# Kernel optimization log

Hardware: AMD Instinct MI355X
Metric: run time of the kernel (lower is better)

## Reference

```python
import jax, jax.numpy as jnp
import numpy as np

N, K, E = 20000, 4, 320000
IN_DIM, H_IN, D = 1024, 256, 128
GATE_IN = 2 * D + 1  # [h || m || logdeg]
GATE_H = 128         # max(d_out, 32)
TEMP = 0.6
M_CLAMP = 20.0


def _init(key, shape, fan_in):
    return jax.random.normal(key, shape, dtype=jnp.float32) / np.sqrt(fan_in)


def setup_inputs() -> dict:
    key = jax.random.key(0)
    ks = jax.random.split(key, 24)
    inp = {}
    inp['X'] = jax.random.normal(ks[0], (N, IN_DIM), dtype=jnp.float32)
    inp['rows'] = jax.random.randint(ks[1], (K, E), 0, N, dtype=jnp.int32)
    inp['cols'] = jax.random.randint(ks[2], (K, E), 0, N, dtype=jnp.int32)
    inp['mask'] = jnp.ones((N, K), dtype=jnp.float32)
    inp['logdeg'] = jax.random.uniform(ks[3], (N, K), dtype=jnp.float32) * 3.0
    # lin_in: 3-layer MLP 1024 -> 256 -> 256 -> 128, each + ReLU
    inp['W_in0'] = _init(ks[4], (IN_DIM, H_IN), IN_DIM); inp['b_in0'] = jnp.zeros((H_IN,), jnp.float32)
    inp['W_in1'] = _init(ks[5], (H_IN, H_IN), H_IN);     inp['b_in1'] = jnp.zeros((H_IN,), jnp.float32)
    inp['W_in2'] = _init(ks[6], (H_IN, D), H_IN);        inp['b_in2'] = jnp.zeros((D,), jnp.float32)
    # block 0
    inp['Wmsg0'] = _init(ks[7], (D, D), D)
    inp['Wg1_0'] = _init(ks[8], (GATE_IN, GATE_H), GATE_IN); inp['bg1_0'] = jnp.zeros((GATE_H,), jnp.float32)
    inp['Wg2_0'] = _init(ks[9], (GATE_H, 1), GATE_H);        inp['bg2_0'] = jnp.zeros((1,), jnp.float32)
    # block 1
    inp['Wmsg1'] = _init(ks[10], (D, D), D)
    inp['Wg1_1'] = _init(ks[11], (GATE_IN, GATE_H), GATE_IN); inp['bg1_1'] = jnp.zeros((GATE_H,), jnp.float32)
    inp['Wg2_1'] = _init(ks[12], (GATE_H, 1), GATE_H);        inp['bg2_1'] = jnp.zeros((1,), jnp.float32)
    # head
    inp['Wh1'] = _init(ks[13], (D, D), D); inp['bh1'] = jnp.zeros((D,), jnp.float32)
    inp['Wh2'] = _init(ks[14], (D, 1), D); inp['bh2'] = jnp.zeros((1,), jnp.float32)
    return inp


def reference(X, rows, cols, mask, logdeg,
              W_in0, b_in0, W_in1, b_in1, W_in2, b_in2,
              Wmsg0, Wg1_0, bg1_0, Wg2_0, bg2_0,
              Wmsg1, Wg1_1, bg1_1, Wg2_1, bg2_1,
              Wh1, bh1, Wh2, bh2):
    relu = jax.nn.relu
    # input encoder (eval mode: dropout / featdrop are identity)
    H = relu(relu(relu(X @ W_in0 + b_in0) @ W_in1 + b_in1) @ W_in2 + b_in2)

    def pairnorm(x):
        x = x - x.mean(axis=0, keepdims=True)
        mean_norm = jnp.sqrt(jnp.mean(jnp.sum(x * x, axis=1))) + 1e-6
        return x / mean_norm

    def block(H, Wmsg, Wg1, bg1, Wg2, bg2):
        Z = H @ Wmsg  # [N, D]
        def prop(r, c):  # sparse A_k @ Z with binary adjacency: out[r] += Z[c]
            return jax.ops.segment_sum(Z[c], r, num_segments=N)
        M = jnp.transpose(jax.vmap(prop)(rows, cols), (1, 0, 2))  # [N, K, D]
        M = jnp.clip(M, -M_CLAMP, M_CLAMP)
        H_rep = jnp.broadcast_to(H[:, None, :], (N, K, H.shape[1]))
        gate_in = jnp.concatenate([H_rep, M, logdeg[:, :, None]], axis=2)  # [N, K, 2D+1]
        scores = (relu(gate_in @ Wg1 + bg1) @ Wg2 + bg2)[..., 0]  # [N, K]
        alpha = jax.nn.softmax(scores / TEMP, axis=1)
        alpha = alpha * mask
        alpha = alpha / jnp.maximum(alpha.sum(axis=1, keepdims=True), 1e-12)
        alpha = jnp.maximum(alpha, 1e-8)
        alpha = alpha / jnp.maximum(alpha.sum(axis=1, keepdims=True), 1e-12)
        fused = jnp.einsum('nk,nkd->nd', alpha, M)
        return fused, alpha

    fused0, a0 = block(H, Wmsg0, Wg1_0, bg1_0, Wg2_0, bg2_0)
    H = relu(pairnorm(fused0 + H))
    fused1, a1 = block(H, Wmsg1, Wg1_1, bg1_1, Wg2_1, bg2_1)
    H = relu(pairnorm(fused1 + H))

    h = relu(relu(H) @ Wh1 + bh1)
    logits = (h @ Wh2 + bh2)[:, 0]  # [N]
    return logits, jnp.stack([a0, a1], axis=0)
```

## Files before the change

### kernel.cpp

```cpp
#include <hip/hip_runtime.h>
#include <hip/hip_bf16.h>

#define N_NODES 20000
#define KADJ 4
#define NEDGE 320000
#define ETOTAL (KADJ * NEDGE)
#define IN_DIM_ 1024
#define H_IN_ 256
#define DDIM 128
#define GATE_H_ 128
#define TEMP_ 0.6f
#define M_CLAMP_ 20.0f
#define CSR_TOTAL (KADJ * N_NODES)
#define NCOARSE 128
#define QPER (CSR_TOTAL / NCOARSE)
#define ESTRIDE 12288
#define TILE_A 4096
#define BINA_NB ((ETOTAL + TILE_A - 1) / TILE_A)

typedef __attribute__((ext_vector_type(8))) short frag_ab;
typedef __attribute__((ext_vector_type(4))) float frag_cd;
typedef __attribute__((ext_vector_type(8))) unsigned short us8;

__device__ inline unsigned short f2bf(float f) {
    unsigned int u = __float_as_uint(f);
    u += 0x7FFFu + ((u >> 16) & 1);
    return (unsigned short)(u >> 16);
}
__device__ inline float bflo(unsigned int p) { return __uint_as_float(p << 16); }
__device__ inline float bfhi(unsigned int p) { return __uint_as_float(p & 0xffff0000u); }

__device__ __forceinline__ void gld16(const unsigned short* g, unsigned short* l) {
    __builtin_amdgcn_global_load_lds(
        (const __attribute__((address_space(1))) void*)g,
        (__attribute__((address_space(3))) void*)l, 16, 0, 0);
}

__global__ __launch_bounds__(256) void cast_bf16_kernel(
    const float* __restrict__ X, unsigned short* __restrict__ Xb, int n)
{
    int i = (blockIdx.x * 256 + threadIdx.x) * 8;
    if (i >= n) return;
    float4 a = *(const float4*)(X + i), b = *(const float4*)(X + i + 4);
    us8 o;
    o[0] = f2bf(a.x); o[1] = f2bf(a.y); o[2] = f2bf(a.z); o[3] = f2bf(a.w);
    o[4] = f2bf(b.x); o[5] = f2bf(b.y); o[6] = f2bf(b.z); o[7] = f2bf(b.w);
    *(us8*)(Xb + i) = o;
}

#define PIPE_WAIT_NEXT()  asm volatile("s_waitcnt vmcnt(5)" ::: "memory")
#define PIPE_WAIT_LAST()  asm volatile("s_waitcnt vmcnt(0)" ::: "memory")
#define PIPE_BAR()        __builtin_amdgcn_s_barrier()
#define PIPE_FENCE()      __builtin_amdgcn_sched_barrier(0)


__global__ __launch_bounds__(256) void gemm_async_kernel(
    const unsigned short* __restrict__ A, const unsigned short* __restrict__ Bt,
    const float* __restrict__ bias, float* __restrict__ Cf, unsigned short* __restrict__ Cb,
    int M, int N, int K, int do_relu)
{
    __shared__ unsigned short sA[2][32 * 64];
    __shared__ unsigned short sB[2][128 * 64];
    int tid = threadIdx.x;
    int tileM = blockIdx.y * 32, tileN = blockIdx.x * 128;
    int w = tid >> 6, lane = tid & 63;
    int wr = (w & 1) * 16, wc = (w >> 1) * 64;
    int fm = lane & 15, fq = lane >> 4;
    int crow = lane >> 3;
    int gsw = (lane & 7) ^ crow;

    frag_cd acc[4] = {};

    auto stage = [&](int buf, int k0) {
        {
            int row = w * 8 + crow;
            int ar = min(tileM + row, M - 1);
            gld16(A + (size_t)ar * K + k0 + gsw * 8, &sA[buf][w * 512]);
        }
#pragma unroll
        for (int t = 0; t < 4; t++) {
            int chunk = w * 4 + t;
            int row = chunk * 8 + crow;
            gld16(Bt + (size_t)(tileN + row) * K + k0 + gsw * 8, &sB[buf][chunk * 512]);
        }
    };

    int nt = K >> 6;
    stage(0, 0);
    for (int t = 0; t < nt; t++) {
        int cur = t & 1;
        if (t + 1 < nt) { stage(cur ^ 1, (t + 1) << 6); PIPE_WAIT_NEXT(); }
        else            { PIPE_WAIT_LAST(); }
        PIPE_BAR();
        PIPE_FENCE();
#pragma unroll
        for (int s = 0; s < 2; s++) {
            int sw = ((s * 4 + fq) ^ (fm & 7)) * 8;
            frag_ab af = *(const frag_ab*)&sA[cur][(wr + fm) * 64 + sw];
#pragma unroll
            for (int j = 0; j < 4; j++) {
                frag_ab bf = *(const frag_ab*)&sB[cur][(wc + j * 16 + fm) * 64 + sw];
                acc[j] = __builtin_amdgcn_mfma_f32_16x16x32_bf16(af, bf, acc[j], 0, 0, 0);
            }
        }
        PIPE_FENCE();
        PIPE_BAR();
    }
    int row = tileM + wr + fq * 4;
#pragma unroll
    for (int r = 0; r < 4; r++) {
        if (row + r < M) {
#pragma unroll
            for (int j = 0; j < 4; j++) {
                int col = tileN + wc + j * 16 + fm;
                float v = acc[j][r];
                if (bias) v += bias[col];
                if (do_relu) v = fmaxf(v, 0.f);
                if (Cf) Cf[(size_t)(row + r) * N + col] = v;
                if (Cb) Cb[(size_t)(row + r) * N + col] = f2bf(v);
            }
        }
    }
}

__global__ __launch_bounds__(256) void zg_gemm_kernel(
    const unsigned short* __restrict__ A, const unsigned short* __restrict__ Bt,
    const float* __restrict__ bg1, unsigned short* __restrict__ Zb,
    float* __restrict__ GH, int M)
{
    __shared__ unsigned short sA[2][32 * 64];
    __shared__ unsigned short sB[2][128 * 64];
    int tid = threadIdx.x;
    int tileM = blockIdx.y * 32, tileN = blockIdx.x * 128;
    int w = tid >> 6, lane = tid & 63;
    int wr = (w & 1) * 16, wc = (w >> 1) * 64;
    int fm = lane & 15, fq = lane >> 4;
    int crow = lane >> 3;
    int gsw = (lane & 7) ^ crow;

    frag_cd acc[4] = {};

    auto stage = [&](int buf, int k0) {
        {
            int row = w * 8 + crow;
            int ar = min(tileM + row, M - 1);
            gld16(A + (size_t)ar * DDIM + k0 + gsw * 8, &sA[buf][w * 512]);
        }
#pragma unroll
        for (int t = 0; t < 4; t++) {
            int chunk = w * 4 + t;
            int row = chunk * 8 + crow;
            gld16(Bt + (size_t)(tileN + row) * DDIM + k0 + gsw * 8, &sB[buf][chunk * 512]);
        }
    };

    stage(0, 0);
#pragma unroll
    for (int t = 0; t < 2; t++) {
        int cur = t & 1;
        if (t == 0) { stage(1, 64); PIPE_WAIT_NEXT(); }
        else        { PIPE_WAIT_LAST(); }
        PIPE_BAR();
        PIPE_FENCE();
#pragma unroll
        for (int s = 0; s < 2; s++) {
            int sw = ((s * 4 + fq) ^ (fm & 7)) * 8;
            frag_ab af = *(const frag_ab*)&sA[cur][(wr + fm) * 64 + sw];
#pragma unroll
            for (int j = 0; j < 4; j++) {
                frag_ab bf = *(const frag_ab*)&sB[cur][(wc + j * 16 + fm) * 64 + sw];
                acc[j] = __builtin_amdgcn_mfma_f32_16x16x32_bf16(af, bf, acc[j], 0, 0, 0);
            }
        }
        PIPE_FENCE();
        PIPE_BAR();
    }
    int isZ = (blockIdx.x == 0);
    int row = tileM + wr + fq * 4;
#pragma unroll
    for (int r = 0; r < 4; r++) {
        if (row + r < M) {
#pragma unroll
            for (int j = 0; j < 4; j++) {
                int col = wc + j * 16 + fm;
                float v = acc[j][r];
                if (isZ) Zb[(size_t)(row + r) * DDIM + col] = f2bf(v);
                else     GH[(size_t)(row + r) * GATE_H_ + col] = v + bg1[col];
            }
        }
    }
}

__global__ __launch_bounds__(256) void head_gemm_kernel(
    const unsigned short* __restrict__ A, const unsigned short* __restrict__ Bt,
    const float* __restrict__ bh1, const float* __restrict__ Wh2,
    const float* __restrict__ bh2, float* __restrict__ logits, int M)
{
    __shared__ unsigned short sA[2][32 * 64];
    __shared__ unsigned short sB[2][128 * 64];
    __shared__ float sred[2][32];
    int tid = threadIdx.x;
    int tileM = blockIdx.x * 32;
    int w = tid >> 6, lane = tid & 63;
    int wr = (w & 1) * 16, wc = (w >> 1) * 64;
    int fm = lane & 15, fq = lane >> 4;
    int crow = lane >> 3;
    int gsw = (lane & 7) ^ crow;

    frag_cd acc[4] = {};

    auto stage = [&](int buf, int k0) {
        {
            int row = w * 8 + crow;
            int ar = min(tileM + row, M - 1);
            gld16(A + (size_t)ar * DDIM + k0 + gsw * 8, &sA[buf][w * 512]);
        }
#pragma unroll
        for (int t = 0; t < 4; t++) {
            int chunk = w * 4 + t;
            int row = chunk * 8 + crow;
            gld16(Bt + (size_t)row * DDIM + k0 + gsw * 8, &sB[buf][chunk * 512]);
        }
    };

    stage(0, 0);
#pragma unroll
    for (int t = 0; t < 2; t++) {
        int cur = t & 1;
        if (t == 0) { stage(1, 64); PIPE_WAIT_NEXT(); }
        else        { PIPE_WAIT_LAST(); }
        PIPE_BAR();
        PIPE_FENCE();
#pragma unroll
        for (int s = 0; s < 2; s++) {
            int sw = ((s * 4 + fq) ^ (fm & 7)) * 8;
            frag_ab af = *(const frag_ab*)&sA[cur][(wr + fm) * 64 + sw];
#pragma unroll
            for (int j = 0; j < 4; j++) {
                frag_ab bf = *(const frag_ab*)&sB[cur][(wc + j * 16 + fm) * 64 + sw];
                acc[j] = __builtin_amdgcn_mfma_f32_16x16x32_bf16(af, bf, acc[j], 0, 0, 0);
            }
        }
        PIPE_FENCE();
        PIPE_BAR();
    }
    float wv[4], bh[4];
#pragma unroll
    for (int j = 0; j < 4; j++) {
        int c = wc + j * 16 + fm;
        wv[j] = Wh2[c];
        bh[j] = bh1[c];
    }
    float part[4];
#pragma unroll
    for (int r = 0; r < 4; r++) {
        float p = 0.f;
#pragma unroll
        for (int j = 0; j < 4; j++) {
            float v = fmaxf(acc[j][r] + bh[j], 0.f);
            p += v * wv[j];
        }
        part[r] = p;
    }
#pragma unroll
    for (int m = 1; m < 16; m <<= 1)
#pragma unroll
        for (int r = 0; r < 4; r++)
            part[r] += __shfl_xor(part[r], m, 64);
    if (fm == 0) {
#pragma unroll
        for (int r = 0; r < 4; r++)
            sred[w >> 1][wr + fq * 4 + r] = part[r];
    }
    __syncthreads();
    if (tid < 32 && tileM + tid < M)
        logits[tileM + tid] = sred[0][tid] + sred[1][tid] + bh2[0];
}

__global__ __launch_bounds__(256) void gate_gemm_kernel(
    const unsigned short* __restrict__ Mb, const unsigned short* __restrict__ Bt,
    const float* __restrict__ GH, const float* __restrict__ logdeg,
    const float* __restrict__ wld, const float* __restrict__ Wg2,
    const float* __restrict__ bg2, float* __restrict__ scores)
{
    __shared__ unsigned short sA[2][32 * 64];
    __shared__ unsigned short sB[2][128 * 64];
    __shared__ float sred[2][32];
    int tid = threadIdx.x;
    int tile0 = blockIdx.x * 32;
    int w = tid >> 6, lane = tid & 63;
    int wr = (w & 1) * 16, wc = (w >> 1) * 64;
    int fm = lane & 15, fq = lane >> 4;
    int crow = lane >> 3;
    int gsw = (lane & 7) ^ crow;

    frag_cd acc[4] = {};

    auto stage = [&](int buf, int k0) {
        {
            int row = w * 8 + crow;
            gld16(Mb + (size_t)(tile0 + row) * DDIM + k0 + gsw * 8, &sA[buf][w * 512]);
        }
#pragma unroll
        for (int t = 0; t < 4; t++) {
            int chunk = w * 4 + t;
            int row = chunk * 8 + crow;
            gld16(Bt + (size_t)row * DDIM + k0 + gsw * 8, &sB[buf][chunk * 512]);
        }
    };

    stage(0, 0);
#pragma unroll
    for (int t = 0; t < 2; t++) {
        int cur = t & 1;
        if (t == 0) { stage(1, 64); PIPE_WAIT_NEXT(); }
        else        { PIPE_WAIT_LAST(); }
        PIPE_BAR();
        PIPE_FENCE();
#pragma unroll
        for (int s = 0; s < 2; s++) {
            int sw = ((s * 4 + fq) ^ (fm & 7)) * 8;
            frag_ab af = *(const frag_ab*)&sA[cur][(wr + fm) * 64 + sw];
#pragma unroll
            for (int j = 0; j < 4; j++) {
                frag_ab bf = *(const frag_ab*)&sB[cur][(wc + j * 16 + fm) * 64 + sw];
                acc[j] = __builtin_amdgcn_mfma_f32_16x16x32_bf16(af, bf, acc[j], 0, 0, 0);
            }
        }
        PIPE_FENCE();
        PIPE_BAR();
    }
    float wg2v[4], wldv[4];
#pragma unroll
    for (int j = 0; j < 4; j++) {
        int c = wc + j * 16 + fm;
        wg2v[j] = Wg2[c];
        wldv[j] = wld[c];
    }
    float part[4];
#pragma unroll
    for (int r = 0; r < 4; r++) {
        int q = tile0 + wr + fq * 4 + r;
        int n = q >> 2;
        float ld = logdeg[q];
        float p = 0.f;
#pragma unroll
        for (int j = 0; j < 4; j++) {
            int c = wc + j * 16 + fm;
            float v = acc[j][r] + GH[(size_t)n * GATE_H_ + c] + ld * wldv[j];
            p += fmaxf(v, 0.f) * wg2v[j];
        }
        part[r] = p;
    }
#pragma unroll
    for (int m = 1; m < 16; m <<= 1)
#pragma unroll
        for (int r = 0; r < 4; r++)
            part[r] += __shfl_xor(part[r], m, 64);
    if (fm == 0) {
#pragma unroll
        for (int r = 0; r < 4; r++)
            sred[w >> 1][wr + fq * 4 + r] = part[r];
    }
    __syncthreads();
    if (tid < 32) scores[tile0 + tid] = sred[0][tid] + sred[1][tid] + bg2[0];
}

struct TD { const float* src; unsigned short* dst; int K; int N; };
struct TD10 { TD d[10]; };

__global__ __launch_bounds__(256) void transpose_all_kernel(TD10 descs)
{
    TD t = descs.d[blockIdx.z];
    int n0 = blockIdx.x * 32, k0 = blockIdx.y * 32;
    if (n0 >= t.N || k0 >= t.K) return;
    __shared__ float tile[32][33];
    int tx = threadIdx.x & 31, ty4 = (threadIdx.x >> 5) * 4;
#pragma unroll
    for (int i = 0; i < 4; i++)
        tile[ty4 + i][tx] = t.src[(size_t)(k0 + ty4 + i) * t.N + n0 + tx];
    __syncthreads();
#pragma unroll
    for (int i = 0; i < 4; i++)
        t.dst[(size_t)(n0 + ty4 + i) * t.K + k0 + tx] = f2bf(tile[tx][ty4 + i]);
}

__global__ __launch_bounds__(256) void binA2_kernel(
    const int* __restrict__ rows, const int* __restrict__ cols,
    int* __restrict__ bcnt, uint2* __restrict__ staging)
{
    __shared__ int hist[NCOARSE], hscan[NCOARSE], lcur[NCOARSE], gbase[NCOARSE];
    __shared__ uint2 pairs[TILE_A];
    int tid = threadIdx.x;
    int base = blockIdx.x * TILE_A;
    int cnt_t = min(TILE_A, ETOTAL - base);

    for (int i = tid; i < NCOARSE; i += 256) hist[i] = 0;
    __syncthreads();

    unsigned int q[16], c[16];
    bool valid[16];
#pragma unroll
    for (int i = 0; i < 16; i++) {
        int loc = i * 256 + tid;
        valid[i] = loc < cnt_t;
        if (valid[i]) {
            int e = base + loc;
            int k = e / NEDGE;
            unsigned int qq = (unsigned int)(k * N_NODES + rows[e]);
            q[i] = qq;
            c[i] = (unsigned int)cols[e];
            atomicAdd(&hist[qq / QPER], 1);
        }
    }
    __syncthreads();
    if (tid < NCOARSE) hscan[tid] = hist[tid];
    __syncthreads();
    for (int d = 1; d < NCOARSE; d <<= 1) {
        int v = (tid >= d && tid < NCOARSE) ? hscan[tid - d] : 0;
        __syncthreads();
        if (tid < NCOARSE) hscan[tid] += v;
        __syncthreads();
    }
    if (tid < NCOARSE) {
        int ex = hscan[tid] - hist[tid];
        hscan[tid] = ex;
        lcur[tid] = ex;
        gbase[tid] = hist[tid] ? (tid * ESTRIDE + atomicAdd(&bcnt[tid], hist[tid])) : 0;
    }
    __syncthreads();
#pragma unroll
    for (int i = 0; i < 16; i++) {
        if (valid[i]) {
            int b = q[i] / QPER;
            int p = atomicAdd(&lcur[b], 1);
            pairs[p] = make_uint2(q[i], c[i]);
        }
    }
    __syncthreads();
    for (int i = tid; i < cnt_t; i += 256) {
        uint2 pr = pairs[i];
        int b = pr.x / QPER;
        staging[gbase[b] + (i - hscan[b])] = pr;
    }
}

__global__ __launch_bounds__(256) void binB2_kernel(
    const uint2* __restrict__ staging, const int* __restrict__ bcnt,
    int* __restrict__ offs, int* __restrict__ ends, int* __restrict__ edst)
{
    __shared__ int cntS[QPER], sofs[QPER], lcur[QPER];
    __shared__ int psum[256];
    int tid = threadIdx.x, b = blockIdx.x;
    int q0 = b * QPER, base = b * ESTRIDE;
    int fill = bcnt[b];
    for (int i = tid; i < QPER; i += 256) cntS[i] = 0;
    __syncthreads();
    for (int i = tid; i < fill; i += 256)
        atomicAdd(&cntS[staging[base + i].x - q0], 1);
    __syncthreads();
    const int CH = 3;
    int lo = tid * CH, hi = min(lo + CH, QPER);
    int s = 0;
    for (int i = lo; i < hi; i++) s += cntS[i];
    psum[tid] = s;
    __syncthreads();
    for (int d = 1; d < 256; d <<= 1) {
        int v = (tid >= d) ? psum[tid - d] : 0;
        __syncthreads();
        psum[tid] += v;
        __syncthreads();
    }
    int run = (tid == 0) ? 0 : psum[tid - 1];
    for (int i = lo; i < hi; i++) {
        sofs[i] = run;
        lcur[i] = run;
        run += cntS[i];
    }
    __syncthreads();
    for (int i = tid; i < QPER; i += 256) {
        offs[q0 + i] = base + sofs[i];
        ends[q0 + i] = base + sofs[i] + cntS[i];
    }
    for (int i = tid; i < fill; i += 256) {
        uint2 p = staging[base + i];
        int pos = atomicAdd(&lcur[p.x - q0], 1);
        edst[base + pos] = (int)p.y;
    }
}

__global__ __launch_bounds__(256) void gather_kernel(
    const int* __restrict__ offs, const int* __restrict__ ends,
    const int* __restrict__ edst,
    const unsigned short* __restrict__ Zb, unsigned short* __restrict__ Mb)
{
    int q = blockIdx.x * 4 + (threadIdx.x >> 6);
    int lane = threadIdx.x & 63;
    int qw = lane >> 4;
    int l = lane & 15;
    int k = q / N_NODES;
    int r = q - k * N_NODES;
    int start = offs[q];
    int end = ends[q];

    float a0 = 0.f, a1 = 0.f, a2 = 0.f, a3 = 0.f;
    float a4 = 0.f, a5 = 0.f, a6 = 0.f, a7 = 0.f;

#define ACC8(P) {                                  \
        a0 += bflo(P.x); a1 += bfhi(P.x);          \
        a2 += bflo(P.y); a3 += bfhi(P.y);          \
        a4 += bflo(P.z); a5 += bfhi(P.z);          \
        a6 += bflo(P.w); a7 += bfhi(P.w); }

    int i = start + qw;
    for (; i + 12 < end; i += 16) {
        int c0 = edst[i], c1 = edst[i + 4], c2 = edst[i + 8], c3 = edst[i + 12];
        uint4 p0 = *(const uint4*)(Zb + (size_t)c0 * DDIM + l * 8);
        uint4 p1 = *(const uint4*)(Zb + (size_t)c1 * DDIM + l * 8);
        uint4 p2 = *(const uint4*)(Zb + (size_t)c2 * DDIM + l * 8);
        uint4 p3 = *(const uint4*)(Zb + (size_t)c3 * DDIM + l * 8);
        ACC8(p0); ACC8(p1); ACC8(p2); ACC8(p3);
    }
    for (; i + 4 < end; i += 8) {
        int c0 = edst[i], c1 = edst[i + 4];
        uint4 p0 = *(const uint4*)(Zb + (size_t)c0 * DDIM + l * 8);
        uint4 p1 = *(const uint4*)(Zb + (size_t)c1 * DDIM + l * 8);
        ACC8(p0); ACC8(p1);
    }
    if (i < end) {
        int c0 = edst[i];
        uint4 p0 = *(const uint4*)(Zb + (size_t)c0 * DDIM + l * 8);
        ACC8(p0);
    }
#undef ACC8

#define QRED(x) { x += __shfl_xor(x, 16, 64); x += __shfl_xor(x, 32, 64); }
    QRED(a0) QRED(a1) QRED(a2) QRED(a3) QRED(a4) QRED(a5) QRED(a6) QRED(a7)
#undef QRED

#define CLIP(v) fminf(fmaxf(v, -M_CLAMP_), M_CLAMP_)
    unsigned int w0 = (unsigned int)f2bf(CLIP(a0)) | ((unsigned int)f2bf(CLIP(a1)) << 16);
    unsigned int w1 = (unsigned int)f2bf(CLIP(a2)) | ((unsigned int)f2bf(CLIP(a3)) << 16);
    unsigned int w2 = (unsigned int)f2bf(CLIP(a4)) | ((unsigned int)f2bf(CLIP(a5)) << 16);
    unsigned int w3 = (unsigned int)f2bf(CLIP(a6)) | ((unsigned int)f2bf(CLIP(a7)) << 16);
#undef CLIP
    if (qw == 0) {
        uint4 o = make_uint4(w0, w1, w2, w3);
        *(uint4*)(Mb + ((size_t)r * KADJ + k) * DDIM + l * 8) = o;
    }
}

__global__ __launch_bounds__(256) void fuse_kernel(
    const unsigned short* __restrict__ Mb, const float* __restrict__ scores,
    const float* __restrict__ mask, const float* __restrict__ H,
    float* __restrict__ Y, float* __restrict__ alpha_out, float* __restrict__ red, int N)
{
    int tid = threadIdx.x;
    int sub = tid >> 6;
    int j = tid & 63;
    int dd = j * 2;
    float csx = 0.f, csy = 0.f, sq = 0.f;

    for (int t = blockIdx.x; t < N / 4; t += gridDim.x) {
        int n = t * 4 + sub;
        float a[KADJ];
        float mx = -1e30f;
#pragma unroll
        for (int k = 0; k < KADJ; k++) {
            a[k] = scores[(size_t)n * KADJ + k] * (1.0f / TEMP_);
            mx = fmaxf(mx, a[k]);
        }
        float sum = 0.f;
#pragma unroll
        for (int k = 0; k < KADJ; k++) { a[k] = expf(a[k] - mx); sum += a[k]; }
#pragma unroll
        for (int k = 0; k < KADJ; k++) a[k] = (a[k] / sum) * mask[(size_t)n * KADJ + k];
        float s2 = 0.f;
#pragma unroll
        for (int k = 0; k < KADJ; k++) s2 += a[k];
        float inv = 1.f / fmaxf(s2, 1e-12f);
#pragma unroll
        for (int k = 0; k < KADJ; k++) a[k] = fmaxf(a[k] * inv, 1e-8f);
        s2 = 0.f;
#pragma unroll
        for (int k = 0; k < KADJ; k++) s2 += a[k];
        inv = 1.f / fmaxf(s2, 1e-12f);
#pragma unroll
        for (int k = 0; k < KADJ; k++) a[k] *= inv;

        float2 h = *(const float2*)(H + (size_t)n * DDIM + dd);
        float yx = h.x, yy = h.y;
#pragma unroll
        for (int k = 0; k < KADJ; k++) {
            unsigned int u = *(const unsigned int*)(Mb + ((size_t)n * KADJ + k) * DDIM + dd);
            yx += a[k] * bflo(u);
            yy += a[k] * bfhi(u);
        }
        *(float2*)(Y + (size_t)n * DDIM + dd) = make_float2(yx, yy);
        if (j < KADJ) alpha_out[(size_t)n * KADJ + j] = a[j];
        csx += yx; csy += yy;
        sq += yx * yx + yy * yy;
    }

    __shared__ float sx[256], sy[256], sq_[256];
    sx[tid] = csx; sy[tid] = csy; sq_[tid] = sq;
    __syncthreads();
    if (tid < 64) {
        float ax = sx[tid] + sx[tid + 64] + sx[tid + 128] + sx[tid + 192];
        float ay = sy[tid] + sy[tid + 64] + sy[tid + 128] + sy[tid + 192];
        atomicAdd(&red[tid * 2], ax);
        atomicAdd(&red[tid * 2 + 1], ay);
    }
    for (int s = 128; s > 0; s >>= 1) {
        if (tid < s) sq_[tid] += sq_[tid + s];
        __syncthreads();
    }
    if (tid == 0) atomicAdd(&red[128], sq_[0]);
}

__global__ __launch_bounds__(256) void pairnorm_kernel(
    const float* __restrict__ Y, const float* __restrict__ red,
    float* __restrict__ Hout, unsigned short* __restrict__ Hb, int N)
{
    int tid = threadIdx.x;
    int d = tid & 127;
    float invN = 1.0f / (float)N;
    float mu = red[d] * invN;
    __shared__ float smu2[128];
    if (tid < 128) smu2[tid] = mu * mu;
    __syncthreads();
    for (int s = 64; s > 0; s >>= 1) {
        if (tid < s) smu2[tid] += smu2[tid + s];
        __syncthreads();
    }
    float summu2 = smu2[0];
    float var = red[128] * invN - summu2;
    float norm = sqrtf(fmaxf(var, 0.f)) + 1e-6f;
    float inv = 1.0f / norm;
    int n = blockIdx.x * 2 + (tid >> 7);
    if (n < N) {
        float v = (Y[(size_t)n * DDIM + d] - mu) * inv;
        v = fmaxf(v, 0.f);
        Hout[(size_t)n * DDIM + d] = v;
        Hb[(size_t)n * DDIM + d] = f2bf(v);
    }
}

extern "C" void kernel_launch(void* const* d_in, const int* in_sizes, int n_in,
                              void* d_out, int out_size, void* d_ws, size_t ws_size,
                              hipStream_t stream)
{
    const float* X      = (const float*)d_in[0];
    const int*   rows   = (const int*)d_in[1];
    const int*   cols   = (const int*)d_in[2];
    const float* mask   = (const float*)d_in[3];
    const float* logdeg = (const float*)d_in[4];
    const float* W_in0  = (const float*)d_in[5];
    const float* b_in0  = (const float*)d_in[6];
    const float* W_in1  = (const float*)d_in[7];
    const float* b_in1  = (const float*)d_in[8];
    const float* W_in2  = (const float*)d_in[9];
    const float* b_in2  = (const float*)d_in[10];
    const float* Wmsg[2] = {(const float*)d_in[11], (const float*)d_in[16]};
    const float* Wg1[2]  = {(const float*)d_in[12], (const float*)d_in[17]};
    const float* bg1[2]  = {(const float*)d_in[13], (const float*)d_in[18]};
    const float* Wg2[2]  = {(const float*)d_in[14], (const float*)d_in[19]};
    const float* bg2[2]  = {(const float*)d_in[15], (const float*)d_in[20]};
    const float* Wh1 = (const float*)d_in[21];
    const float* bh1 = (const float*)d_in[22];
    const float* Wh2 = (const float*)d_in[23];
    const float* bh2 = (const float*)d_in[24];

    float* ws = (float*)d_ws;
    unsigned short* Xb  = (unsigned short*)ws;
    unsigned short* Mb  = (unsigned short*)ws;
    float* Ybuf  = ws + 5120000;
    float* GH    = ws + 7680000;
    uint2* staging = (uint2*)(ws + 10240000);
    unsigned short* H0b = (unsigned short*)(ws + 10240000);
    unsigned short* H1b = (unsigned short*)(ws + 12800000);
    unsigned short* Zb  = (unsigned short*)(ws + 12800000);
    float* H     = ws + 15360000;
    unsigned short* Hb = (unsigned short*)(ws + 17920000);
    float* scores = ws + 19200000;
    int*   offs   = (int*)(ws + 19280000);
    int*   ends   = (int*)(ws + 19360000);
    int*   edst   = (int*)(ws + 19440000);
    int*   bcnt   = (int*)(ws + 21013120);
    unsigned short* w0t  = (unsigned short*)(ws + 21013248);
    unsigned short* w1t  = (unsigned short*)(ws + 21144320);
    unsigned short* w2t  = (unsigned short*)(ws + 21177088);
    unsigned short* wzg[2]  = {(unsigned short*)(ws + 21193472), (unsigned short*)(ws + 21209856)};
    unsigned short* wgmt[2] = {(unsigned short*)(ws + 21226240), (unsigned short*)(ws + 21234432)};
    unsigned short* wh1t = (unsigned short*)(ws + 21242624);
    float* red    = ws + 21250816;
    float* logits = (float*)d_out;
    float* alpha_out = (float*)d_out + N_NODES;

    dim3 blk(256);
    int gM32 = (N_NODES + 31) / 32;

    (void)hipMemsetAsync(bcnt, 0, NCOARSE * sizeof(int), stream);
    (void)hipMemsetAsync(red, 0, 260 * sizeof(float), stream);
    binA2_kernel<<<BINA_NB, blk, 0, stream>>>(rows, cols, bcnt, staging);
    binB2_kernel<<<NCOARSE, blk, 0, stream>>>(staging, bcnt, offs, ends, edst);

    TD10 descs;
    descs.d[0] = {W_in0, w0t, IN_DIM_, H_IN_};
    descs.d[1] = {W_in1, w1t, H_IN_, H_IN_};
    descs.d[2] = {W_in2, w2t, H_IN_, DDIM};
    descs.d[3] = {Wmsg[0], wzg[0], DDIM, DDIM};
    descs.d[4] = {Wg1[0], wzg[0] + DDIM * DDIM, DDIM, GATE_H_};
    descs.d[5] = {Wmsg[1], wzg[1], DDIM, DDIM};
    descs.d[6] = {Wg1[1], wzg[1] + DDIM * DDIM, DDIM, GATE_H_};
    descs.d[7] = {Wg1[0] + DDIM * GATE_H_, wgmt[0], DDIM, GATE_H_};
    descs.d[8] = {Wg1[1] + DDIM * GATE_H_, wgmt[1], DDIM, GATE_H_};
    descs.d[9] = {Wh1, wh1t, DDIM, DDIM};
    transpose_all_kernel<<<dim3(8, 32, 10), blk, 0, stream>>>(descs);
    cast_bf16_kernel<<<N_NODES * IN_DIM_ / 8 / 256, blk, 0, stream>>>(X, Xb, N_NODES * IN_DIM_);

    gemm_async_kernel<<<dim3(2, gM32), blk, 0, stream>>>(Xb, w0t, b_in0, nullptr, H0b, N_NODES, H_IN_, IN_DIM_, 1);
    gemm_async_kernel<<<dim3(2, gM32), blk, 0, stream>>>(H0b, w1t, b_in1, nullptr, H1b, N_NODES, H_IN_, H_IN_, 1);
    gemm_async_kernel<<<dim3(1, gM32), blk, 0, stream>>>(H1b, w2t, b_in2, H, Hb, N_NODES, DDIM, H_IN_, 1);

    for (int b = 0; b < 2; b++) {
        zg_gemm_kernel<<<dim3(2, gM32), blk, 0, stream>>>(Hb, wzg[b], bg1[b], Zb, GH, N_NODES);
        gather_kernel<<<CSR_TOTAL / 4, blk, 0, stream>>>(offs, ends, edst, Zb, Mb);
        gate_gemm_kernel<<<CSR_TOTAL / 32, blk, 0, stream>>>(Mb, wgmt[b], GH, logdeg,
                                                             Wg1[b] + 256 * GATE_H_, Wg2[b], bg2[b], scores);
        float* alph = alpha_out + (size_t)b * N_NODES * KADJ;
        fuse_kernel<<<512, blk, 0, stream>>>(Mb, scores, mask, H, Ybuf, alph, red + b * 130, N_NODES);
        pairnorm_kernel<<<(N_NODES + 1) / 2, blk, 0, stream>>>(Ybuf, red + b * 130, H, Hb, N_NODES);
    }

    head_gemm_kernel<<<gM32, blk, 0, stream>>>(Hb, wh1t, bh1, Wh2, bh2, logits, N_NODES);
}
```

Measured before the change: 491.1 us.

## Merge prep kernels and fuse gate scoring with softmax-weighted fusion

Three prep kernels (bf16 cast of X, weight transposes, edge binning phase A) become one launch that dispatches on block index. The gate GEMM kernel now also does the per-node softmax/mask normalisation, the alpha-weighted sum over the K adjacency messages plus residual, and the pairnorm partial sums, so the scores buffer round-trip and the separate fuse kernel go away. Pairnorm reduction atomics are spread across 8 stripes to cut contention, and the two memsets become one. The cost is one atomic set per 8-node block instead of per persistent block, and a heavier gate kernel epilogue.

New measurement: 456.7 us. -7.0%, faster.

```diff
diff --git a/kernel.cpp b/kernel.cpp
--- a/kernel.cpp
+++ b/kernel.cpp
@@ -17,6 +17,8 @@
 #define ESTRIDE 12288
 #define TILE_A 4096
 #define BINA_NB ((ETOTAL + TILE_A - 1) / TILE_A)
+#define NB_CAST (N_NODES * IN_DIM_ / 8 / 256)
+#define NB_TRANS 2560
 
 typedef __attribute__((ext_vector_type(8))) short frag_ab;
 typedef __attribute__((ext_vector_type(4))) float frag_cd;
@@ -36,23 +38,109 @@
         (__attribute__((address_space(3))) void*)l, 16, 0, 0);
 }
 
-__global__ __launch_bounds__(256) void cast_bf16_kernel(
-    const float* __restrict__ X, unsigned short* __restrict__ Xb, int n)
-{
-    int i = (blockIdx.x * 256 + threadIdx.x) * 8;
-    if (i >= n) return;
-    float4 a = *(const float4*)(X + i), b = *(const float4*)(X + i + 4);
-    us8 o;
-    o[0] = f2bf(a.x); o[1] = f2bf(a.y); o[2] = f2bf(a.z); o[3] = f2bf(a.w);
-    o[4] = f2bf(b.x); o[5] = f2bf(b.y); o[6] = f2bf(b.z); o[7] = f2bf(b.w);
-    *(us8*)(Xb + i) = o;
-}
-
 #define PIPE_WAIT_NEXT()  asm volatile("s_waitcnt vmcnt(5)" ::: "memory")
 #define PIPE_WAIT_LAST()  asm volatile("s_waitcnt vmcnt(0)" ::: "memory")
 #define PIPE_BAR()        __builtin_amdgcn_s_barrier()
 #define PIPE_FENCE()      __builtin_amdgcn_sched_barrier(0)
 
+
+struct TD { const float* src; unsigned short* dst; int K; int N; };
+struct TD10 { TD d[10]; };
+
+__global__ __launch_bounds__(256) void prep_kernel(
+    const float* __restrict__ X, unsigned short* __restrict__ Xb,
+    TD10 descs,
+    const int* __restrict__ rows, const int* __restrict__ cols,
+    int* __restrict__ bcnt, uint2* __restrict__ staging)
+{
+    __shared__ __align__(16) char sraw[2048 + TILE_A * 8];
+    int bid = blockIdx.x;
+    int tid = threadIdx.x;
+
+    if (bid < NB_CAST) {
+        int i = (bid * 256 + tid) * 8;
+        float4 a = *(const float4*)(X + i), b = *(const float4*)(X + i + 4);
+        us8 o;
+        o[0] = f2bf(a.x); o[1] = f2bf(a.y); o[2] = f2bf(a.z); o[3] = f2bf(a.w);
+        o[4] = f2bf(b.x); o[5] = f2bf(b.y); o[6] = f2bf(b.z); o[7] = f2bf(b.w);
+        *(us8*)(Xb + i) = o;
+        return;
+    }
+    if (bid < NB_CAST + NB_TRANS) {
+        int b2 = bid - NB_CAST;
+        TD t = descs.d[b2 >> 8];
+        int rem = b2 & 255;
+        int n0 = (rem & 7) * 32, k0 = (rem >> 3) * 32;
+        if (n0 >= t.N || k0 >= t.K) return;
+        float (*tile)[33] = (float(*)[33])sraw;
+        int tx = tid & 31, ty4 = (tid >> 5) * 4;
+#pragma unroll
+        for (int i = 0; i < 4; i++)
+            tile[ty4 + i][tx] = t.src[(size_t)(k0 + ty4 + i) * t.N + n0 + tx];
+        __syncthreads();
+#pragma unroll
+        for (int i = 0; i < 4; i++)
+            t.dst[(size_t)(n0 + ty4 + i) * t.K + k0 + tx] = f2bf(tile[tx][ty4 + i]);
+        return;
+    }
+    int* hist  = (int*)sraw;
+    int* hscan = hist + NCOARSE;
+    int* lcur  = hscan + NCOARSE;
+    int* gbase = lcur + NCOARSE;
+    uint2* pairs = (uint2*)(sraw + 2048);
+
+    int base = (bid - NB_CAST - NB_TRANS) * TILE_A;
+    int cnt_t = min(TILE_A, ETOTAL - base);
+
+    for (int i = tid; i < NCOARSE; i += 256) hist[i] = 0;
+    __syncthreads();
+
+    unsigned int q[16], c[16];
+    bool valid[16];
+#pragma unroll
+    for (int i = 0; i < 16; i++) {
+        int loc = i * 256 + tid;
+        valid[i] = loc < cnt_t;
+        if (valid[i]) {
+            int e = base + loc;
+            int k = e / NEDGE;
+            unsigned int qq = (unsigned int)(k * N_NODES + rows[e]);
+            q[i] = qq;
+            c[i] = (unsigned int)cols[e];
+            atomicAdd(&hist[qq / QPER], 1);
+        }
+    }
+    __syncthreads();
+    if (tid < NCOARSE) hscan[tid] = hist[tid];
+    __syncthreads();
+    for (int d = 1; d < NCOARSE; d <<= 1) {
+        int v = (tid >= d && tid < NCOARSE) ? hscan[tid - d] : 0;
+        __syncthreads();
+        if (tid < NCOARSE) hscan[tid] += v;
+        __syncthreads();
+    }
+    if (tid < NCOARSE) {
+        int ex = hscan[tid] - hist[tid];
+        hscan[tid] = ex;
+        lcur[tid] = ex;
+        gbase[tid] = hist[tid] ? (tid * ESTRIDE + atomicAdd(&bcnt[tid], hist[tid])) : 0;
+    }
+    __syncthreads();
+#pragma unroll
+    for (int i = 0; i < 16; i++) {
+        if (valid[i]) {
+            int b = q[i] / QPER;
+            int p = atomicAdd(&lcur[b], 1);
+            pairs[p] = make_uint2(q[i], c[i]);
+        }
+    }
+    __syncthreads();
+    for (int i = tid; i < cnt_t; i += 256) {
+        uint2 pr = pairs[i];
+        int b = pr.x / QPER;
+        staging[gbase[b] + (i - hscan[b])] = pr;
+    }
+}
 
 __global__ __launch_bounds__(256) void gemm_async_kernel(
     const unsigned short* __restrict__ A, const unsigned short* __restrict__ Bt,
@@ -277,17 +365,22 @@
         logits[tileM + tid] = sred[0][tid] + sred[1][tid] + bh2[0];
 }
 
-__global__ __launch_bounds__(256) void gate_gemm_kernel(
+__global__ __launch_bounds__(256) void gate_fuse_kernel(
     const unsigned short* __restrict__ Mb, const unsigned short* __restrict__ Bt,
     const float* __restrict__ GH, const float* __restrict__ logdeg,
     const float* __restrict__ wld, const float* __restrict__ Wg2,
-    const float* __restrict__ bg2, float* __restrict__ scores)
+    const float* __restrict__ bg2, const float* __restrict__ mask,
+    const float* __restrict__ H, float* __restrict__ Y,
+    float* __restrict__ alpha_out, float* __restrict__ red)
 {
     __shared__ unsigned short sA[2][32 * 64];
     __shared__ unsigned short sB[2][128 * 64];
     __shared__ float sred[2][32];
+    __shared__ float sc_al[64];
+    __shared__ float sx[256], sy[256], sqs[256];
     int tid = threadIdx.x;
     int tile0 = blockIdx.x * 32;
+    int node0 = blockIdx.x * 8;
     int w = tid >> 6, lane = tid & 63;
     int wr = (w & 1) * 16, wc = (w >> 1) * 64;
     int fm = lane & 15, fq = lane >> 4;
@@ -363,86 +456,70 @@
             sred[w >> 1][wr + fq * 4 + r] = part[r];
     }
     __syncthreads();
-    if (tid < 32) scores[tile0 + tid] = sred[0][tid] + sred[1][tid] + bg2[0];
-}
-
-struct TD { const float* src; unsigned short* dst; int K; int N; };
-struct TD10 { TD d[10]; };
-
-__global__ __launch_bounds__(256) void transpose_all_kernel(TD10 descs)
-{
-    TD t = descs.d[blockIdx.z];
-    int n0 = blockIdx.x * 32, k0 = blockIdx.y * 32;
-    if (n0 >= t.N || k0 >= t.K) return;
-    __shared__ float tile[32][33];
-    int tx = threadIdx.x & 31, ty4 = (threadIdx.x >> 5) * 4;
-#pragma unroll
-    for (int i = 0; i < 4; i++)
-        tile[ty4 + i][tx] = t.src[(size_t)(k0 + ty4 + i) * t.N + n0 + tx];
-    __syncthreads();
-#pragma unroll
-    for (int i = 0; i < 4; i++)
-        t.dst[(size_t)(n0 + ty4 + i) * t.K + k0 + tx] = f2bf(tile[tx][ty4 + i]);
-}
-
-__global__ __launch_bounds__(256) void binA2_kernel(
-    const int* __restrict__ rows, const int* __restrict__ cols,
-    int* __restrict__ bcnt, uint2* __restrict__ staging)
-{
-    __shared__ int hist[NCOARSE], hscan[NCOARSE], lcur[NCOARSE], gbase[NCOARSE];
-    __shared__ uint2 pairs[TILE_A];
-    int tid = threadIdx.x;
-    int base = blockIdx.x * TILE_A;
-    int cnt_t = min(TILE_A, ETOTAL - base);
-
-    for (int i = tid; i < NCOARSE; i += 256) hist[i] = 0;
-    __syncthreads();
-
-    unsigned int q[16], c[16];
-    bool valid[16];
-#pragma unroll
-    for (int i = 0; i < 16; i++) {
-        int loc = i * 256 + tid;
-        valid[i] = loc < cnt_t;
-        if (valid[i]) {
-            int e = base + loc;
-            int k = e / NEDGE;
-            unsigned int qq = (unsigned int)(k * N_NODES + rows[e]);
-            q[i] = qq;
-            c[i] = (unsigned int)cols[e];
-            atomicAdd(&hist[qq / QPER], 1);
-        }
-    }
-    __syncthreads();
-    if (tid < NCOARSE) hscan[tid] = hist[tid];
-    __syncthreads();
-    for (int d = 1; d < NCOARSE; d <<= 1) {
-        int v = (tid >= d && tid < NCOARSE) ? hscan[tid - d] : 0;
+    if (tid < 32) sc_al[tid] = sred[0][tid] + sred[1][tid] + bg2[0];
+    __syncthreads();
+    if (tid < 8) {
+        int n = node0 + tid;
+        float a[KADJ];
+        float mx = -1e30f;
+#pragma unroll
+        for (int k = 0; k < KADJ; k++) {
+            a[k] = sc_al[tid * 4 + k] * (1.0f / TEMP_);
+            mx = fmaxf(mx, a[k]);
+        }
+        float sum = 0.f;
+#pragma unroll
+        for (int k = 0; k < KADJ; k++) { a[k] = expf(a[k] - mx); sum += a[k]; }
+#pragma unroll
+        for (int k = 0; k < KADJ; k++) a[k] = (a[k] / sum) * mask[(size_t)n * KADJ + k];
+        float s2 = 0.f;
+#pragma unroll
+        for (int k = 0; k < KADJ; k++) s2 += a[k];
+        float inv = 1.f / fmaxf(s2, 1e-12f);
+#pragma unroll
+        for (int k = 0; k < KADJ; k++) a[k] = fmaxf(a[k] * inv, 1e-8f);
+        s2 = 0.f;
+#pragma unroll
+        for (int k = 0; k < KADJ; k++) s2 += a[k];
+        inv = 1.f / fmaxf(s2, 1e-12f);
+#pragma unroll
+        for (int k = 0; k < KADJ; k++) sc_al[32 + tid * 4 + k] = a[k] * inv;
+    }
+    __syncthreads();
+    if (tid < 32) alpha_out[tile0 + tid] = sc_al[32 + tid];
+    float csx = 0.f, csy = 0.f, sq = 0.f;
+    int j = tid & 63, dd = j * 2;
+#pragma unroll
+    for (int it = 0; it < 2; it++) {
+        int nl = (tid >> 6) + it * 4;
+        int n = node0 + nl;
+        const float* alp = &sc_al[32 + nl * 4];
+        float2 h = *(const float2*)(H + (size_t)n * DDIM + dd);
+        float yx = h.x, yy = h.y;
+#pragma unroll
+        for (int k = 0; k < KADJ; k++) {
+            unsigned int u = *(const unsigned int*)(Mb + ((size_t)n * KADJ + k) * DDIM + dd);
+            yx += alp[k] * bflo(u);
+            yy += alp[k] * bfhi(u);
+        }
+        *(float2*)(Y + (size_t)n * DDIM + dd) = make_float2(yx, yy);
+        csx += yx; csy += yy;
+        sq += yx * yx + yy * yy;
+    }
+    sx[tid] = csx; sy[tid] = csy; sqs[tid] = sq;
+    __syncthreads();
+    int st = (blockIdx.x & 7) * 132;
+    if (tid < 64) {
+        float ax = sx[tid] + sx[tid + 64] + sx[tid + 128] + sx[tid + 192];
+        float ay = sy[tid] + sy[tid + 64] + sy[tid + 128] + sy[tid + 192];
+        atomicAdd(&red[st + tid * 2], ax);
+        atomicAdd(&red[st + tid * 2 + 1], ay);
+    }
+    for (int s = 128; s > 0; s >>= 1) {
+        if (tid < s) sqs[tid] += sqs[tid + s];
         __syncthreads();
-        if (tid < NCOARSE) hscan[tid] += v;
-        __syncthreads();
-    }
-    if (tid < NCOARSE) {
-        int ex = hscan[tid] - hist[tid];
-        hscan[tid] = ex;
-        lcur[tid] = ex;
-        gbase[tid] = hist[tid] ? (tid * ESTRIDE + atomicAdd(&bcnt[tid], hist[tid])) : 0;
-    }
-    __syncthreads();
-#pragma unroll
-    for (int i = 0; i < 16; i++) {
-        if (valid[i]) {
-            int b = q[i] / QPER;
-            int p = atomicAdd(&lcur[b], 1);
-            pairs[p] = make_uint2(q[i], c[i]);
-        }
-    }
-    __syncthreads();
-    for (int i = tid; i < cnt_t; i += 256) {
-        uint2 pr = pairs[i];
-        int b = pr.x / QPER;
-        staging[gbase[b] + (i - hscan[b])] = pr;
-    }
+    }
+    if (tid == 0) atomicAdd(&red[st + 128], sqs[0]);
 }
 
 __global__ __launch_bounds__(256) void binB2_kernel(
@@ -550,74 +627,6 @@
     }
 }
 
-__global__ __launch_bounds__(256) void fuse_kernel(
-    const unsigned short* __restrict__ Mb, const float* __restrict__ scores,
-    const float* __restrict__ mask, const float* __restrict__ H,
-    float* __restrict__ Y, float* __restrict__ alpha_out, float* __restrict__ red, int N)
-{
-    int tid = threadIdx.x;
-    int sub = tid >> 6;
-    int j = tid & 63;
-    int dd = j * 2;
-    float csx = 0.f, csy = 0.f, sq = 0.f;
-
-    for (int t = blockIdx.x; t < N / 4; t += gridDim.x) {
-        int n = t * 4 + sub;
-        float a[KADJ];
-        float mx = -1e30f;
-#pragma unroll
-        for (int k = 0; k < KADJ; k++) {
-            a[k] = scores[(size_t)n * KADJ + k] * (1.0f / TEMP_);
-            mx = fmaxf(mx, a[k]);
-        }
-        float sum = 0.f;
-#pragma unroll
-        for (int k = 0; k < KADJ; k++) { a[k] = expf(a[k] - mx); sum += a[k]; }
-#pragma unroll
-        for (int k = 0; k < KADJ; k++) a[k] = (a[k] / sum) * mask[(size_t)n * KADJ + k];
-        float s2 = 0.f;
-#pragma unroll
-        for (int k = 0; k < KADJ; k++) s2 += a[k];
-        float inv = 1.f / fmaxf(s2, 1e-12f);
-#pragma unroll
-        for (int k = 0; k < KADJ; k++) a[k] = fmaxf(a[k] * inv, 1e-8f);
-        s2 = 0.f;
-#pragma unroll
-        for (int k = 0; k < KADJ; k++) s2 += a[k];
-        inv = 1.f / fmaxf(s2, 1e-12f);
-#pragma unroll
-        for (int k = 0; k < KADJ; k++) a[k] *= inv;
-
-        float2 h = *(const float2*)(H + (size_t)n * DDIM + dd);
-        float yx = h.x, yy = h.y;
-#pragma unroll
-        for (int k = 0; k < KADJ; k++) {
-            unsigned int u = *(const unsigned int*)(Mb + ((size_t)n * KADJ + k) * DDIM + dd);
-            yx += a[k] * bflo(u);
-            yy += a[k] * bfhi(u);
-        }
-        *(float2*)(Y + (size_t)n * DDIM + dd) = make_float2(yx, yy);
-        if (j < KADJ) alpha_out[(size_t)n * KADJ + j] = a[j];
-        csx += yx; csy += yy;
-        sq += yx * yx + yy * yy;
-    }
-
-    __shared__ float sx[256], sy[256], sq_[256];
-    sx[tid] = csx; sy[tid] = csy; sq_[tid] = sq;
-    __syncthreads();
-    if (tid < 64) {
-        float ax = sx[tid] + sx[tid + 64] + sx[tid + 128] + sx[tid + 192];
-        float ay = sy[tid] + sy[tid + 64] + sy[tid + 128] + sy[tid + 192];
-        atomicAdd(&red[tid * 2], ax);
-        atomicAdd(&red[tid * 2 + 1], ay);
-    }
-    for (int s = 128; s > 0; s >>= 1) {
-        if (tid < s) sq_[tid] += sq_[tid + s];
-        __syncthreads();
-    }
-    if (tid == 0) atomicAdd(&red[128], sq_[0]);
-}
-
 __global__ __launch_bounds__(256) void pairnorm_kernel(
     const float* __restrict__ Y, const float* __restrict__ red,
     float* __restrict__ Hout, unsigned short* __restrict__ Hb, int N)
@@ -625,16 +634,22 @@
     int tid = threadIdx.x;
     int d = tid & 127;
     float invN = 1.0f / (float)N;
-    float mu = red[d] * invN;
+    float s = 0.f, rq = 0.f;
+#pragma unroll
+    for (int st = 0; st < 8; st++) {
+        s += red[st * 132 + d];
+        rq += red[st * 132 + 128];
+    }
+    float mu = s * invN;
     __shared__ float smu2[128];
     if (tid < 128) smu2[tid] = mu * mu;
     __syncthreads();
-    for (int s = 64; s > 0; s >>= 1) {
-        if (tid < s) smu2[tid] += smu2[tid + s];
+    for (int t = 64; t > 0; t >>= 1) {
+        if (tid < t) smu2[tid] += smu2[tid + t];
         __syncthreads();
     }
     float summu2 = smu2[0];
-    float var = red[128] * invN - summu2;
+    float var = rq * invN - summu2;
     float norm = sqrtf(fmaxf(var, 0.f)) + 1e-6f;
     float inv = 1.0f / norm;
     int n = blockIdx.x * 2 + (tid >> 7);
@@ -682,28 +697,24 @@
     unsigned short* Zb  = (unsigned short*)(ws + 12800000);
     float* H     = ws + 15360000;
     unsigned short* Hb = (unsigned short*)(ws + 17920000);
-    float* scores = ws + 19200000;
+    int*   bcnt  = (int*)(ws + 19200000);
+    float* red   = ws + 19200128;
     int*   offs   = (int*)(ws + 19280000);
     int*   ends   = (int*)(ws + 19360000);
     int*   edst   = (int*)(ws + 19440000);
-    int*   bcnt   = (int*)(ws + 21013120);
     unsigned short* w0t  = (unsigned short*)(ws + 21013248);
     unsigned short* w1t  = (unsigned short*)(ws + 21144320);
     unsigned short* w2t  = (unsigned short*)(ws + 21177088);
     unsigned short* wzg[2]  = {(unsigned short*)(ws + 21193472), (unsigned short*)(ws + 21209856)};
     unsigned short* wgmt[2] = {(unsigned short*)(ws + 21226240), (unsigned short*)(ws + 21234432)};
     unsigned short* wh1t = (unsigned short*)(ws + 21242624);
-    float* red    = ws + 21250816;
     float* logits = (float*)d_out;
     float* alpha_out = (float*)d_out + N_NODES;
 
     dim3 blk(256);
     int gM32 = (N_NODES + 31) / 32;
 
-    (void)hipMemsetAsync(bcnt, 0, NCOARSE * sizeof(int), stream);
-    (void)hipMemsetAsync(red, 0, 260 * sizeof(float), stream);
-    binA2_kernel<<<BINA_NB, blk, 0, stream>>>(rows, cols, bcnt, staging);
-    binB2_kernel<<<NCOARSE, blk, 0, stream>>>(staging, bcnt, offs, ends, edst);
+    (void)hipMemsetAsync(bcnt, 0, (128 + 2 * 8 * 132) * sizeof(float), stream);
 
     TD10 descs;
     descs.d[0] = {W_in0, w0t, IN_DIM_, H_IN_};
@@ -716,8 +727,9 @@
     descs.d[7] = {Wg1[0] + DDIM * GATE_H_, wgmt[0], DDIM, GATE_H_};
     descs.d[8] = {Wg1[1] + DDIM * GATE_H_, wgmt[1], DDIM, GATE_H_};
     descs.d[9] = {Wh1, wh1t, DDIM, DDIM};
-    transpose_all_kernel<<<dim3(8, 32, 10), blk, 0, stream>>>(descs);
-    cast_bf16_kernel<<<N_NODES * IN_DIM_ / 8 / 256, blk, 0, stream>>>(X, Xb, N_NODES * IN_DIM_);
+    prep_kernel<<<NB_CAST + NB_TRANS + BINA_NB, blk, 0, stream>>>(
+        X, Xb, descs, rows, cols, bcnt, staging);
+    binB2_kernel<<<NCOARSE, blk, 0, stream>>>(staging, bcnt, offs, ends, edst);
 
     gemm_async_kernel<<<dim3(2, gM32), blk, 0, stream>>>(Xb, w0t, b_in0, nullptr, H0b, N_NODES, H_IN_, IN_DIM_, 1);
     gemm_async_kernel<<<dim3(2, gM32), blk, 0, stream>>>(H0b, w1t, b_in1, nullptr, H1b, N_NODES, H_IN_, H_IN_, 1);
@@ -726,11 +738,11 @@
     for (int b = 0; b < 2; b++) {
         zg_gemm_kernel<<<dim3(2, gM32), blk, 0, stream>>>(Hb, wzg[b], bg1[b], Zb, GH, N_NODES);
         gather_kernel<<<CSR_TOTAL / 4, blk, 0, stream>>>(offs, ends, edst, Zb, Mb);
-        gate_gemm_kernel<<<CSR_TOTAL / 32, blk, 0, stream>>>(Mb, wgmt[b], GH, logdeg,
-                                                             Wg1[b] + 256 * GATE_H_, Wg2[b], bg2[b], scores);
         float* alph = alpha_out + (size_t)b * N_NODES * KADJ;
-        fuse_kernel<<<512, blk, 0, stream>>>(Mb, scores, mask, H, Ybuf, alph, red + b * 130, N_NODES);
-        pairnorm_kernel<<<(N_NODES + 1) / 2, blk, 0, stream>>>(Ybuf, red + b * 130, H, Hb, N_NODES);
+        gate_fuse_kernel<<<CSR_TOTAL / 32, blk, 0, stream>>>(
+            Mb, wgmt[b], GH, logdeg, Wg1[b] + 256 * GATE_H_, Wg2[b], bg2[b],
+            mask, H, Ybuf, alph, red + b * 8 * 132);
+        pairnorm_kernel<<<(N_NODES + 1) / 2, blk, 0, stream>>>(Ybuf, red + b * 8 * 132, H, Hb, N_NODES);
     }
 
     head_gemm_kernel<<<gM32, blk, 0, stream>>>(Hb, wh1t, bh1, Wh2, bh2, logits, N_NODES);
```
